# Kernel optimization log

Hardware: AMD Instinct MI355X
Metric: run time of the kernel (lower is better)

The kernel has to match this reference:

```python
import math
import jax, jax.numpy as jnp
import numpy as np

B, S, HID = 1, 2048, 2880
H, HKV, D = 64, 8, 64
G = H // HKV  # num_key_value_groups = 8


def setup_inputs() -> dict:
    key = jax.random.key(0)
    ks = jax.random.split(key, 10)
    sd = 1.0 / math.sqrt(HID)
    hidden_states = jax.random.normal(ks[0], (B, S, HID), dtype=jnp.float32)
    # causal additive mask [B, 1, S, S]
    causal = jnp.tril(jnp.ones((S, S), dtype=bool))
    attention_mask = jnp.where(causal, 0.0, -1e9).astype(jnp.float32)[None, None]
    Wq = jax.random.normal(ks[1], (H * D, HID), dtype=jnp.float32) * sd
    bq = jax.random.normal(ks[2], (H * D,), dtype=jnp.float32) * 0.01
    Wk = jax.random.normal(ks[3], (HKV * D, HID), dtype=jnp.float32) * sd
    bk = jax.random.normal(ks[4], (HKV * D,), dtype=jnp.float32) * 0.01
    Wv = jax.random.normal(ks[5], (HKV * D, HID), dtype=jnp.float32) * sd
    bv = jax.random.normal(ks[6], (HKV * D,), dtype=jnp.float32) * 0.01
    Wo = jax.random.normal(ks[7], (HID, H * D), dtype=jnp.float32) * (1.0 / math.sqrt(H * D))
    bo = jax.random.normal(ks[8], (HID,), dtype=jnp.float32) * 0.01
    return {"hidden_states": hidden_states, "attention_mask": attention_mask,
            "Wq": Wq, "bq": bq, "Wk": Wk, "bk": bk, "Wv": Wv, "bv": bv,
            "Wo": Wo, "bo": bo}


def reference(hidden_states, attention_mask, Wq, bq, Wk, bk, Wv, bv, Wo, bo):
    b, s, _ = hidden_states.shape
    # projections
    q = hidden_states @ Wq.T + bq  # [b, s, H*D]
    k = hidden_states @ Wk.T + bk  # [b, s, HKV*D]
    v = hidden_states @ Wv.T + bv
    # torch q head index h maps to kv head h // G, so split H -> (HKV, G)
    q = q.reshape(b, s, HKV, G, D).transpose(0, 2, 3, 1, 4)   # [b, kv, g, s, d]
    k = k.reshape(b, s, HKV, D).transpose(0, 2, 1, 3)         # [b, kv, s, d]
    v = v.reshape(b, s, HKV, D).transpose(0, 2, 1, 3)
    # grouped-query attention without materializing repeated KV (same math as repeat_interleave)
    scores = jnp.einsum('bkgsd,bktd->bkgst', q, k) / math.sqrt(D)
    scores = scores + attention_mask[:, :, None]              # broadcast [b,1,1,s,t]
    attn = jax.nn.softmax(scores.astype(jnp.float32), axis=-1).astype(q.dtype)
    out = jnp.einsum('bkgst,bktd->bkgsd', attn, v)            # [b, kv, g, s, d]
    out = out.transpose(0, 3, 1, 2, 4).reshape(b, s, H * D)
    return out @ Wo.T + bo
```

## Files before the change

### kernel.cpp

```cpp
#include <hip/hip_runtime.h>
#include <hip/hip_bf16.h>
#include <cmath>

typedef __hip_bfloat16 bf16;
typedef __bf16 bf16x8 __attribute__((ext_vector_type(8)));
typedef float floatx4 __attribute__((ext_vector_type(4)));

__device__ inline floatx4 mfma16(bf16x8 a, bf16x8 b, floatx4 c) {
  return __builtin_amdgcn_mfma_f32_16x16x32_bf16(a, b, c, 0, 0, 0);
}

__device__ inline void async_ld16(const void* g, void* l) {
  __builtin_amdgcn_global_load_lds((const __attribute__((address_space(1))) void*)g,
                                   (__attribute__((address_space(3))) void*)l,
                                   16, 0, 0);
}

__device__ inline uint4 pack8(float4 a, float4 b) {
  union { uint4 u; bf16 h[8]; } t;
  t.h[0] = __float2bfloat16(a.x); t.h[1] = __float2bfloat16(a.y);
  t.h[2] = __float2bfloat16(a.z); t.h[3] = __float2bfloat16(a.w);
  t.h[4] = __float2bfloat16(b.x); t.h[5] = __float2bfloat16(b.y);
  t.h[6] = __float2bfloat16(b.z); t.h[7] = __float2bfloat16(b.w);
  return t.u;
}

__global__ __launch_bounds__(256)
void cvt_f32_bf16(const float* __restrict__ s, bf16* __restrict__ d, int n8) {
  const int i = blockIdx.x * 256 + threadIdx.x;
  if (i >= n8) return;
  const float4 a = ((const float4*)s)[2 * i];
  const float4 b = ((const float4*)s)[2 * i + 1];
  ((uint4*)d)[i] = pack8(a, b);
}

__global__ void concat_bias3(const float* __restrict__ q, const float* __restrict__ k,
                             const float* __restrict__ v, float* __restrict__ o) {
  const int i = blockIdx.x * 256 + threadIdx.x;
  if (i < 4096) o[i] = q[i];
  else if (i < 4608) o[i] = k[i - 4096];
  else o[i] = v[i - 4608];
}

#define QSCALE 0.1803368801111601f

template <int A_BF, int B_BF, int OUT_MODE>
__global__ __launch_bounds__(256)
void gemm_bt_bias(const void* __restrict__ Ap, const void* __restrict__ Bp,
                  const float* __restrict__ bias, void* __restrict__ Cp,
                  void* __restrict__ Cqp, void* __restrict__ Ctp,
                  int M, int N, int K, float qmul) {
  __shared__ __align__(16) bf16 sA[128 * 32];
  __shared__ __align__(16) bf16 sB[128 * 32];
  const int tid  = threadIdx.x;
  const int wave = tid >> 6;
  const int lane = tid & 63;
  const int quad = lane >> 4;
  const int l15  = lane & 15;
  const int bm = blockIdx.y * 128;
  const int bn = blockIdx.x * 128;
  const int wm = (wave & 1) * 64;
  const int wn = (wave >> 1) * 64;

  floatx4 acc[4][4] = {};

  const int g0 = tid, g1 = tid + 256;
  const int arow0 = bm + (g0 >> 2), acol0 = (g0 & 3) * 8;
  const int arow1 = bm + (g1 >> 2), acol1 = (g1 & 3) * 8;
  int brow0 = bn + (g0 >> 2); if (brow0 >= N) brow0 = N - 1;
  int brow1 = bn + (g1 >> 2); if (brow1 >= N) brow1 = N - 1;

  for (int k0 = 0; k0 < K; k0 += 32) {
    __syncthreads();
    if (A_BF) {
      const bf16* A = (const bf16*)Ap;
      async_ld16(A + (size_t)arow0 * K + k0 + acol0, sA + wave * 512);
      async_ld16(A + (size_t)arow1 * K + k0 + acol1, sA + 2048 + wave * 512);
    } else {
      const float* A = (const float*)Ap;
      const float* p0 = A + (size_t)arow0 * K + k0 + acol0;
      const float* p1 = A + (size_t)arow1 * K + k0 + acol1;
      *(uint4*)(sA + tid * 8)        = pack8(*(const float4*)p0, *(const float4*)(p0 + 4));
      *(uint4*)(sA + 2048 + tid * 8) = pack8(*(const float4*)p1, *(const float4*)(p1 + 4));
    }
    if (B_BF) {
      const bf16* B = (const bf16*)Bp;
      async_ld16(B + (size_t)brow0 * K + k0 + acol0, sB + wave * 512);
      async_ld16(B + (size_t)brow1 * K + k0 + acol1, sB + 2048 + wave * 512);
    } else {
      const float* B = (const float*)Bp;
      const float* p0 = B + (size_t)brow0 * K + k0 + acol0;
      const float* p1 = B + (size_t)brow1 * K + k0 + acol1;
      *(uint4*)(sB + tid * 8)        = pack8(*(const float4*)p0, *(const float4*)(p0 + 4));
      *(uint4*)(sB + 2048 + tid * 8) = pack8(*(const float4*)p1, *(const float4*)(p1 + 4));
    }
    __syncthreads();

    bf16x8 aF[4], bF[4];
#pragma unroll
    for (int mi = 0; mi < 4; ++mi)
      aF[mi] = *(const bf16x8*)(sA + (wm + mi * 16 + l15) * 32 + quad * 8);
#pragma unroll
    for (int ni = 0; ni < 4; ++ni)
      bF[ni] = *(const bf16x8*)(sB + (wn + ni * 16 + l15) * 32 + quad * 8);
#pragma unroll
    for (int mi = 0; mi < 4; ++mi)
#pragma unroll
      for (int ni = 0; ni < 4; ++ni)
        acc[mi][ni] = mfma16(aF[mi], bF[ni], acc[mi][ni]);
  }

#pragma unroll
  for (int ni = 0; ni < 4; ++ni) {
    const int col = bn + wn + ni * 16 + l15;
    if (col >= N) continue;
    const float bv = bias[col];
#pragma unroll
    for (int mi = 0; mi < 4; ++mi) {
      const int row = bm + wm + mi * 16 + quad * 4;
#pragma unroll
      for (int r = 0; r < 4; ++r) {
        const float val = acc[mi][ni][r] + bv;
        if (OUT_MODE == 0) {
          ((bf16*)Cp)[(size_t)(row + r) * N + col] = __float2bfloat16(val * qmul);
        } else if (OUT_MODE == 1) {
          ((float*)Cp)[(size_t)(row + r) * N + col] = val;
        } else if (OUT_MODE == 2) {
          ((bf16*)Ctp)[(size_t)col * M + row + r] = __float2bfloat16(val);
        } else {
          if (col < 4096)      ((bf16*)Cp)[(size_t)(row + r) * 4096 + col] = __float2bfloat16(val * qmul);
          else if (col < 4608) ((bf16*)Cqp)[(size_t)(row + r) * 512 + (col - 4096)] = __float2bfloat16(val);
          else                 ((bf16*)Ctp)[(size_t)(col - 4608) * M + row + r] = __float2bfloat16(val);
        }
      }
    }
  }
}

__global__ __launch_bounds__(256)
void attn_fused(const bf16* __restrict__ Q, const bf16* __restrict__ Kc,
                const bf16* __restrict__ Vt, bf16* __restrict__ AO) {
  constexpr int HD = 4096, KD = 512, SEQ = 2048;
  constexpr float NEG = -1e30f;
  __shared__ __align__(16) bf16 sP[64 * 64];
  __shared__ __align__(16) bf16 sK[2][64 * 64];
  __shared__ __align__(16) bf16 sV[2][64 * 64];

  const int qb = (int)gridDim.x - 1 - blockIdx.x;
  const int h  = blockIdx.y;
  const int kvh = h >> 3;
  const int tid = threadIdx.x, wave = tid >> 6, lane = tid & 63;
  const int quad = lane >> 4, l15 = lane & 15;
  const int sq0 = qb * 64;

  const int lrow = lane >> 3;
  const int lgr  = (lane & 7) ^ lrow;

  bf16x8 qf[2];
#pragma unroll
  for (int ks = 0; ks < 2; ++ks)
    qf[ks] = *(const bf16x8*)(Q + (size_t)(sq0 + wave * 16 + l15) * HD + h * 64 + ks * 32 + quad * 8);

  bf16x8 onesf;
#pragma unroll
  for (int i = 0; i < 8; ++i) onesf[i] = (__bf16)1.0f;

#pragma unroll
  for (int i = 0; i < 2; ++i) {
    const int c = wave * 2 + i;
    async_ld16(Kc + (size_t)(c * 8 + lrow) * KD + kvh * 64 + lgr * 8, &sK[0][c * 512]);
    async_ld16(Vt + (size_t)(kvh * 64 + c * 8 + lrow) * SEQ + lgr * 8, &sV[0][c * 512]);
  }

  floatx4 o_acc[4] = {};
  floatx4 o_sum = {};
  float m_run[4];
#pragma unroll
  for (int r = 0; r < 4; ++r) m_run[r] = NEG;

  for (int kt = 0; kt <= qb; ++kt) {
    const int st0 = kt * 64;
    __syncthreads();

    if (kt < qb) {
      const int st1 = st0 + 64;
      const int nb = (kt + 1) & 1;
#pragma unroll
      for (int i = 0; i < 2; ++i) {
        const int c = wave * 2 + i;
        async_ld16(Kc + (size_t)(st1 + c * 8 + lrow) * KD + kvh * 64 + lgr * 8, &sK[nb][c * 512]);
        async_ld16(Vt + (size_t)(kvh * 64 + c * 8 + lrow) * SEQ + st1 + lgr * 8, &sV[nb][c * 512]);
      }
    }
    const bf16* kb = sK[kt & 1];
    const bf16* vb = sV[kt & 1];

    floatx4 s_acc[4] = {};
#pragma unroll
    for (int ks = 0; ks < 2; ++ks) {
#pragma unroll
      for (int ni = 0; ni < 4; ++ni) {
        const bf16x8 bF = *(const bf16x8*)(kb + (ni * 16 + l15) * 64 + (((ks * 4 + quad) ^ (l15 & 7)) * 8));
        s_acc[ni] = mfma16(qf[ks], bF, s_acc[ni]);
      }
    }

    float x[4][4];
    const int qrow = sq0 + wave * 16 + quad * 4;
#pragma unroll
    for (int ni = 0; ni < 4; ++ni)
#pragma unroll
      for (int r = 0; r < 4; ++r)
        x[ni][r] = s_acc[ni][r];

    if (kt == qb) {
#pragma unroll
      for (int ni = 0; ni < 4; ++ni) {
        const int tcol = st0 + ni * 16 + l15;
#pragma unroll
        for (int r = 0; r < 4; ++r)
          if (tcol > qrow + r) x[ni][r] = NEG;
      }
    }

    float tmax[4] = {NEG, NEG, NEG, NEG};
#pragma unroll
    for (int ni = 0; ni < 4; ++ni)
#pragma unroll
      for (int r = 0; r < 4; ++r)
        tmax[r] = fmaxf(tmax[r], x[ni][r]);
#pragma unroll
    for (int off = 1; off < 16; off <<= 1)
#pragma unroll
      for (int r = 0; r < 4; ++r)
        tmax[r] = fmaxf(tmax[r], __shfl_xor(tmax[r], off));

    const float need = fmaxf(fmaxf(tmax[0] - m_run[0], tmax[1] - m_run[1]),
                             fmaxf(tmax[2] - m_run[2], tmax[3] - m_run[3]));
    if (!__all(need <= 8.0f)) {
#pragma unroll
      for (int r = 0; r < 4; ++r) {
        const float mn = fmaxf(m_run[r], tmax[r]);
        const float alpha = exp2f(m_run[r] - mn);
        m_run[r] = mn;
        o_sum[r] *= alpha;
#pragma unroll
        for (int di = 0; di < 4; ++di)
          o_acc[di][r] *= alpha;
      }
    }

#pragma unroll
    for (int ni = 0; ni < 4; ++ni) {
      const int g = ni * 2 + (l15 >> 3);
      const int c7 = l15 & 7;
#pragma unroll
      for (int r = 0; r < 4; ++r) {
        const int row = wave * 16 + quad * 4 + r;
        sP[row * 64 + ((g ^ (row & 7)) * 8) + c7] =
            __float2bfloat16(exp2f(x[ni][r] - m_run[r]));
      }
    }

#pragma unroll
    for (int ks = 0; ks < 2; ++ks) {
      const bf16x8 aF = *(const bf16x8*)(sP + (wave * 16 + l15) * 64 + (((ks * 4 + quad) ^ (l15 & 7)) * 8));
#pragma unroll
      for (int di = 0; di < 4; ++di) {
        const bf16x8 bF = *(const bf16x8*)(vb + (di * 16 + l15) * 64 + (((ks * 4 + quad) ^ (l15 & 7)) * 8));
        o_acc[di] = mfma16(aF, bF, o_acc[di]);
      }
      o_sum = mfma16(aF, onesf, o_sum);
    }
  }

#pragma unroll
  for (int di = 0; di < 4; ++di) {
    const int col = h * 64 + di * 16 + l15;
#pragma unroll
    for (int r = 0; r < 4; ++r) {
      const int row = sq0 + wave * 16 + quad * 4 + r;
      AO[(size_t)row * HD + col] = __float2bfloat16(o_acc[di][r] / o_sum[r]);
    }
  }
}

extern "C" void kernel_launch(void* const* d_in, const int* in_sizes, int n_in,
                              void* d_out, int out_size, void* d_ws, size_t ws_size,
                              hipStream_t stream) {
  const float* X  = (const float*)d_in[0];
  const float* Wq = (const float*)d_in[2];
  const float* bq = (const float*)d_in[3];
  const float* Wk = (const float*)d_in[4];
  const float* bk = (const float*)d_in[5];
  const float* Wv = (const float*)d_in[6];
  const float* bv = (const float*)d_in[7];
  const float* Wo = (const float*)d_in[8];
  const float* bo = (const float*)d_in[9];
  float* out = (float*)d_out;

  char* ws = (char*)d_ws;
  bf16* Qb = (bf16*)(ws);
  bf16* Kb = (bf16*)(ws + 16777216);
  bf16* Vt = (bf16*)(ws + 18874368);
  bf16* AO = (bf16*)(ws + 20971520);
  bf16*  Xb   = (bf16*)(ws + 37748736);
  bf16*  Wall = (bf16*)(ws + 49545216);
  bf16*  Wob  = (bf16*)(ws + 79036416);
  float* ball = (float*)(ws + 102629376);
  const size_t NEED = 102649856;

  dim3 blk(256);
  if (ws_size >= NEED) {
    cvt_f32_bf16<<<dim3(2048 * 2880 / 8 / 256), blk, 0, stream>>>(X, Xb, 2048 * 2880 / 8);
    cvt_f32_bf16<<<dim3(4096 * 2880 / 8 / 256), blk, 0, stream>>>(Wq, Wall, 4096 * 2880 / 8);
    cvt_f32_bf16<<<dim3(512 * 2880 / 8 / 256),  blk, 0, stream>>>(Wk, Wall + (size_t)4096 * 2880, 512 * 2880 / 8);
    cvt_f32_bf16<<<dim3(512 * 2880 / 8 / 256),  blk, 0, stream>>>(Wv, Wall + (size_t)4608 * 2880, 512 * 2880 / 8);
    cvt_f32_bf16<<<dim3(2880 * 4096 / 8 / 256), blk, 0, stream>>>(Wo, Wob, 2880 * 4096 / 8);
    concat_bias3<<<dim3(20), blk, 0, stream>>>(bq, bk, bv, ball);

    gemm_bt_bias<1, 1, 4><<<dim3(40, 16), blk, 0, stream>>>(Xb, Wall, ball, Qb, Kb, Vt, 2048, 5120, 2880, QSCALE);
    attn_fused<<<dim3(32, 64), blk, 0, stream>>>(Qb, Kb, Vt, AO);
    gemm_bt_bias<1, 1, 1><<<dim3(23, 16), blk, 0, stream>>>(AO, Wob, bo, out, nullptr, nullptr, 2048, 2880, 4096, 1.f);
  } else {
    gemm_bt_bias<0, 0, 0><<<dim3(32, 16), blk, 0, stream>>>(X, Wq, bq, Qb, nullptr, nullptr, 2048, 4096, 2880, QSCALE);
    gemm_bt_bias<0, 0, 0><<<dim3(4, 16),  blk, 0, stream>>>(X, Wk, bk, Kb, nullptr, nullptr, 2048, 512, 2880, 1.f);
    gemm_bt_bias<0, 0, 2><<<dim3(4, 16),  blk, 0, stream>>>(X, Wv, bv, nullptr, nullptr, Vt, 2048, 512, 2880, 1.f);
    attn_fused<<<dim3(32, 64), blk, 0, stream>>>(Qb, Kb, Vt, AO);
    gemm_bt_bias<1, 0, 1><<<dim3(23, 16), blk, 0, stream>>>(AO, Wo, bo, out, nullptr, nullptr, 2048, 2880, 4096, 1.f);
  }
}
```

Before: 551.7 us.

## Transpose attention MFMA operands so each lane owns one query row

Swaps the A/B operands of the QK^T and PV MFMAs so the accumulator holds S^T and O^T, which makes each lane hold a single query row. The row max then needs only two cross-lane shuffles instead of four rounds over four rows, and each lane keeps one running max instead of four. P is written to shared memory as packed 8-byte stores, and the output as packed 4-element bf16 stores with a single reciprocal. The risk is in correctness of the changed mask indexing and the swizzled write layout.

```diff
diff --git a/kernel.cpp b/kernel.cpp
--- a/kernel.cpp
+++ b/kernel.cpp
@@ -174,9 +174,7 @@
 
   floatx4 o_acc[4] = {};
   floatx4 o_sum = {};
-  float m_run[4];
-#pragma unroll
-  for (int r = 0; r < 4; ++r) m_run[r] = NEG;
+  float m_run = NEG;
 
   for (int kt = 0; kt <= qb; ++kt) {
     const int st0 = kt * 64;
@@ -200,88 +198,72 @@
     for (int ks = 0; ks < 2; ++ks) {
 #pragma unroll
       for (int ni = 0; ni < 4; ++ni) {
-        const bf16x8 bF = *(const bf16x8*)(kb + (ni * 16 + l15) * 64 + (((ks * 4 + quad) ^ (l15 & 7)) * 8));
-        s_acc[ni] = mfma16(qf[ks], bF, s_acc[ni]);
+        const bf16x8 kF = *(const bf16x8*)(kb + (ni * 16 + l15) * 64 + (((ks * 4 + quad) ^ (l15 & 7)) * 8));
+        s_acc[ni] = mfma16(kF, qf[ks], s_acc[ni]);
       }
     }
 
-    float x[4][4];
-    const int qrow = sq0 + wave * 16 + quad * 4;
-#pragma unroll
-    for (int ni = 0; ni < 4; ++ni)
+    if (kt == qb) {
+      const int qloc = wave * 16 + l15;
+#pragma unroll
+      for (int ni = 0; ni < 4; ++ni)
+#pragma unroll
+        for (int r = 0; r < 4; ++r)
+          if (ni * 16 + quad * 4 + r > qloc) s_acc[ni][r] = NEG;
+    }
+
+    float t0 = fmaxf(fmaxf(s_acc[0][0], s_acc[0][1]), fmaxf(s_acc[0][2], s_acc[0][3]));
+    float t1 = fmaxf(fmaxf(s_acc[1][0], s_acc[1][1]), fmaxf(s_acc[1][2], s_acc[1][3]));
+    float t2 = fmaxf(fmaxf(s_acc[2][0], s_acc[2][1]), fmaxf(s_acc[2][2], s_acc[2][3]));
+    float t3 = fmaxf(fmaxf(s_acc[3][0], s_acc[3][1]), fmaxf(s_acc[3][2], s_acc[3][3]));
+    float tm = fmaxf(fmaxf(t0, t1), fmaxf(t2, t3));
+    tm = fmaxf(tm, __shfl_xor(tm, 16));
+    tm = fmaxf(tm, __shfl_xor(tm, 32));
+
+    if (!__all(tm - m_run <= 8.0f)) {
+      const float mn = fmaxf(m_run, tm);
+      const float alpha = exp2f(m_run - mn);
+      m_run = mn;
+#pragma unroll
+      for (int r = 0; r < 4; ++r) o_sum[r] *= alpha;
+#pragma unroll
+      for (int di = 0; di < 4; ++di)
+#pragma unroll
+        for (int r = 0; r < 4; ++r) o_acc[di][r] *= alpha;
+    }
+
+    const int prow = wave * 16 + l15;
+#pragma unroll
+    for (int ni = 0; ni < 4; ++ni) {
+      union { uint2 u; bf16 hh[4]; } pk;
 #pragma unroll
       for (int r = 0; r < 4; ++r)
-        x[ni][r] = s_acc[ni][r];
-
-    if (kt == qb) {
-#pragma unroll
-      for (int ni = 0; ni < 4; ++ni) {
-        const int tcol = st0 + ni * 16 + l15;
-#pragma unroll
-        for (int r = 0; r < 4; ++r)
-          if (tcol > qrow + r) x[ni][r] = NEG;
+        pk.hh[r] = __float2bfloat16(exp2f(s_acc[ni][r] - m_run));
+      const int g = ni * 2 + (quad >> 1);
+      *(uint2*)(sP + prow * 64 + ((g ^ (l15 & 7)) * 8) + (quad & 1) * 4) = pk.u;
+    }
+
+#pragma unroll
+    for (int ks = 0; ks < 2; ++ks) {
+      const bf16x8 pF = *(const bf16x8*)(sP + prow * 64 + (((ks * 4 + quad) ^ (l15 & 7)) * 8));
+#pragma unroll
+      for (int di = 0; di < 4; ++di) {
+        const bf16x8 vF = *(const bf16x8*)(vb + (di * 16 + l15) * 64 + (((ks * 4 + quad) ^ (l15 & 7)) * 8));
+        o_acc[di] = mfma16(vF, pF, o_acc[di]);
       }
-    }
-
-    float tmax[4] = {NEG, NEG, NEG, NEG};
-#pragma unroll
-    for (int ni = 0; ni < 4; ++ni)
-#pragma unroll
-      for (int r = 0; r < 4; ++r)
-        tmax[r] = fmaxf(tmax[r], x[ni][r]);
-#pragma unroll
-    for (int off = 1; off < 16; off <<= 1)
-#pragma unroll
-      for (int r = 0; r < 4; ++r)
-        tmax[r] = fmaxf(tmax[r], __shfl_xor(tmax[r], off));
-
-    const float need = fmaxf(fmaxf(tmax[0] - m_run[0], tmax[1] - m_run[1]),
-                             fmaxf(tmax[2] - m_run[2], tmax[3] - m_run[3]));
-    if (!__all(need <= 8.0f)) {
-#pragma unroll
-      for (int r = 0; r < 4; ++r) {
-        const float mn = fmaxf(m_run[r], tmax[r]);
-        const float alpha = exp2f(m_run[r] - mn);
-        m_run[r] = mn;
-        o_sum[r] *= alpha;
-#pragma unroll
-        for (int di = 0; di < 4; ++di)
-          o_acc[di][r] *= alpha;
-      }
-    }
-
-#pragma unroll
-    for (int ni = 0; ni < 4; ++ni) {
-      const int g = ni * 2 + (l15 >> 3);
-      const int c7 = l15 & 7;
-#pragma unroll
-      for (int r = 0; r < 4; ++r) {
-        const int row = wave * 16 + quad * 4 + r;
-        sP[row * 64 + ((g ^ (row & 7)) * 8) + c7] =
-            __float2bfloat16(exp2f(x[ni][r] - m_run[r]));
-      }
-    }
-
-#pragma unroll
-    for (int ks = 0; ks < 2; ++ks) {
-      const bf16x8 aF = *(const bf16x8*)(sP + (wave * 16 + l15) * 64 + (((ks * 4 + quad) ^ (l15 & 7)) * 8));
-#pragma unroll
-      for (int di = 0; di < 4; ++di) {
-        const bf16x8 bF = *(const bf16x8*)(vb + (di * 16 + l15) * 64 + (((ks * 4 + quad) ^ (l15 & 7)) * 8));
-        o_acc[di] = mfma16(aF, bF, o_acc[di]);
-      }
-      o_sum = mfma16(aF, onesf, o_sum);
-    }
-  }
-
+      o_sum = mfma16(onesf, pF, o_sum);
+    }
+  }
+
+  const float inv = 1.0f / o_sum[0];
+  const int row = sq0 + wave * 16 + l15;
 #pragma unroll
   for (int di = 0; di < 4; ++di) {
-    const int col = h * 64 + di * 16 + l15;
-#pragma unroll
-    for (int r = 0; r < 4; ++r) {
-      const int row = sq0 + wave * 16 + quad * 4 + r;
-      AO[(size_t)row * HD + col] = __float2bfloat16(o_acc[di][r] / o_sum[r]);
-    }
+    union { uint2 u; bf16 hh[4]; } pk;
+#pragma unroll
+    for (int r = 0; r < 4; ++r)
+      pk.hh[r] = __float2bfloat16(o_acc[di][r] * inv);
+    *(uint2*)(AO + (size_t)row * HD + h * 64 + di * 16 + quad * 4) = pk.u;
   }
 }
 
```

Result: faster. 513.0 us (-7.0%).
